# Optimization experiments

Measured on AMD Instinct MI355X. Metric: run time of the kernel, lower is better.

## Reference

```python
import jax, jax.numpy as jnp
import numpy as np

N_NODES = 100000
N_EDGES = 1600000


def _graph_conv(num_nodes, edge_index, feat, w, b, in_feats, out_feats):
    src, dst = edge_index[0], edge_index[1]
    # degree of source endpoints, clamp(min=1)^-0.5
    deg = jax.ops.segment_sum(jnp.ones_like(src, dtype=jnp.float32), src, num_segments=num_nodes)
    norm = jnp.power(jnp.clip(deg, 1.0), -0.5)[:, None]  # [N,1]
    feat = feat * norm
    if in_feats > out_feats:
        feat = feat @ w                                   # [N,out]
        rst = jax.ops.segment_sum(feat[src], dst, num_segments=num_nodes)
    else:
        rst = jax.ops.segment_sum(feat[src], dst, num_segments=num_nodes)
        rst = rst @ w
    rst = rst * norm + b
    return jax.nn.relu(rst)


def setup_inputs() -> dict:
    key = jax.random.key(0)
    ks = jax.random.split(key, 8)
    features = jax.random.normal(ks[0], (N_NODES, 256), dtype=jnp.float32)
    e_subgraph = jax.random.randint(ks[1], (2, N_EDGES), 0, N_NODES, dtype=jnp.int64 if jax.config.jax_enable_x64 else jnp.int32)
    n_subgraph = jnp.zeros((N_NODES,), dtype=jnp.int32)
    to_fetch = jax.random.randint(ks[2], (16,), 0, N_NODES, dtype=jnp.int32)
    # GraphConv weights (xavier-like scale), Linear weight (out,in) per F.linear
    w1 = jax.random.normal(ks[3], (256, 128), dtype=jnp.float32) * (2.0 / (256 + 128)) ** 0.5
    b1 = jnp.zeros((128,), dtype=jnp.float32)
    w2 = jax.random.normal(ks[4], (128, 128), dtype=jnp.float32) * (2.0 / (128 + 128)) ** 0.5
    b2 = jnp.zeros((128,), dtype=jnp.float32)
    w3 = jax.random.normal(ks[5], (16, 128), dtype=jnp.float32) * (2.0 / 128) ** 0.5
    b3 = jnp.zeros((16,), dtype=jnp.float32)
    return {"n_subgraph": n_subgraph, "e_subgraph": e_subgraph, "to_fetch": to_fetch,
            "features": features, "w1": w1, "b1": b1, "w2": w2, "b2": b2, "w3": w3, "b3": b3}


def reference(n_subgraph, e_subgraph, to_fetch, features, w1, b1, w2, b2, w3, b3):
    num_nodes = n_subgraph.shape[0]
    h = features.astype(jnp.float32)
    h = _graph_conv(num_nodes, e_subgraph, h, w1, b1, 256, 128)
    h = _graph_conv(num_nodes, e_subgraph, h, w2, b2, 128, 128)
    h = h @ w3.T + b3  # F.linear
    return (h, h)
```

## Files before the change

kernel.cpp:

```cpp
#include <hip/hip_runtime.h>

#define AP 40
#define H2P 136
#define HB 240
#define PB 240
#define NPB 256
#define NBUKMAX 512
#define CAPE 8192

typedef short bf16x8 __attribute__((ext_vector_type(8)));
typedef float f32x4 __attribute__((ext_vector_type(4)));

static __device__ __forceinline__ ushort f2bf(float f) {
  unsigned u = __float_as_uint(f);
  unsigned r = (u + 0x7fffu + ((u >> 16) & 1u)) >> 16;
  return (ushort)r;
}
static __device__ __forceinline__ float bflo(unsigned u) { return __uint_as_float(u << 16); }
static __device__ __forceinline__ float bfhi(unsigned u) { return __uint_as_float(u & 0xffff0000u); }
static __device__ __forceinline__ unsigned packbf(float lo, float hi) {
  return (unsigned)f2bf(lo) | ((unsigned)f2bf(hi) << 16);
}

__global__ __launch_bounds__(256) void k_hist(const int* __restrict__ src, int E,
                                              unsigned* __restrict__ planes, int HW) {
  __shared__ unsigned lds[25600];
  const int per = (E + HB - 1) / HB;
  const int s0 = blockIdx.x * per;
  const int s1 = min(E, s0 + per);
  for (int i = threadIdx.x; i < HW; i += 256) lds[i] = 0u;
  __syncthreads();
  for (int j = s0 + threadIdx.x; j < s1; j += 256) {
    int k = src[j];
    atomicAdd(&lds[k >> 2], 1u << ((k & 3) * 8));
  }
  __syncthreads();
  unsigned* out = planes + (size_t)blockIdx.x * HW;
  for (int i = threadIdx.x; i < HW; i += 256) out[i] = lds[i];
}

__global__ void k_hist_reduce(const unsigned* __restrict__ planes, int HW,
                              float* __restrict__ nrm, int N) {
  int w = blockIdx.x * blockDim.x + threadIdx.x;
  if (w >= HW) return;
  const unsigned* base = planes + w;
  unsigned c0 = 0, c1 = 0, c2 = 0, c3 = 0;
  for (int b = 0; b < HB; b++) {
    unsigned u = base[(size_t)b * HW];
    c0 += u & 255u; c1 += (u >> 8) & 255u; c2 += (u >> 16) & 255u; c3 += u >> 24;
  }
  int n0 = w * 4;
  unsigned c[4] = {c0, c1, c2, c3};
#pragma unroll
  for (int j = 0; j < 4; j++)
    if (n0 + j < N) {
      float d = (float)c[j];
      if (d < 1.f) d = 1.f;
      nrm[n0 + j] = 1.f / sqrtf(d);
    }
}

__global__ __launch_bounds__(256) void k_p0_hist(const int* __restrict__ dst, int E,
                                                 int* __restrict__ hist) {
  __shared__ int cnt[NBUKMAX];
  for (int i = threadIdx.x; i < NBUKMAX; i += 256) cnt[i] = 0;
  __syncthreads();
  const int per = (E + PB - 1) / PB;
  const int s0 = blockIdx.x * per;
  const int s1 = min(E, s0 + per);
  for (int j = s0 + threadIdx.x; j < s1; j += 256)
    atomicAdd(&cnt[dst[j] >> 8], 1);
  __syncthreads();
  for (int i = threadIdx.x; i < NBUKMAX; i += 256) hist[i * PB + blockIdx.x] = cnt[i];
}

__global__ __launch_bounds__(NBUKMAX) void k_p0_scan(int* __restrict__ hist) {
  __shared__ int s[NBUKMAX];
  int b = threadIdx.x;
  const int bi = b * PB;
  int tot = 0;
  for (int blk = 0; blk < PB; blk++) tot += hist[bi + blk];
  s[b] = tot;
  __syncthreads();
  for (int o = 1; o < NBUKMAX; o <<= 1) {
    int x = (b >= o) ? s[b - o] : 0;
    __syncthreads();
    s[b] += x;
    __syncthreads();
  }
  int base = s[b] - tot;
  for (int blk = 0; blk < PB; blk++) {
    int t = hist[bi + blk];
    hist[bi + blk] = base;
    base += t;
  }
}

__global__ __launch_bounds__(256) void k_p1_scatter(const int* __restrict__ src,
                                                    const int* __restrict__ dst, int E,
                                                    const int* __restrict__ hist,
                                                    int2* __restrict__ pairs) {
  __shared__ int cur[NBUKMAX];
  for (int i = threadIdx.x; i < NBUKMAX; i += 256) cur[i] = hist[i * PB + blockIdx.x];
  __syncthreads();
  const int per = (E + PB - 1) / PB;
  const int s0 = blockIdx.x * per;
  const int s1 = min(E, s0 + per);
  for (int j = s0 + threadIdx.x; j < s1; j += 256) {
    int d = dst[j];
    int pos = atomicAdd(&cur[d >> 8], 1);
    pairs[pos] = make_int2(src[j], d);
  }
}

__global__ __launch_bounds__(256) void k_p2_place(const int2* __restrict__ pairs,
                                                  const int* __restrict__ hist,
                                                  int* __restrict__ csr,
                                                  int* __restrict__ row_start,
                                                  int N, int E) {
  __shared__ int stage[CAPE];
  __shared__ int cnt[NPB];
  __shared__ int scn[NPB];
  const int b = blockIdx.x;
  const int t = threadIdx.x;
  const int n0 = b << 8;
  const int n1 = min(N, n0 + NPB);
  const int nn = n1 - n0;
  const int e0 = hist[b * PB];
  const int e1 = hist[(b + 1) * PB];
  for (int i = t; i < nn; i += 256) cnt[i] = 0;
  __syncthreads();
  for (int j = e0 + t; j < e1; j += 256) atomicAdd(&cnt[pairs[j].y - n0], 1);
  __syncthreads();
  int v = (t < nn) ? cnt[t] : 0;
  scn[t] = v;
  __syncthreads();
  for (int o = 1; o < NPB; o <<= 1) {
    int x = (t >= o) ? scn[t - o] : 0;
    __syncthreads();
    scn[t] += x;
    __syncthreads();
  }
  int excl = scn[t] - v;
  if (t < nn) row_start[n0 + t] = e0 + excl;
  if (t == NPB - 1 && n1 == N) row_start[N] = e0 + scn[t];
  __syncthreads();
  if (t < nn) cnt[t] = excl;
  __syncthreads();
  const int seg = e1 - e0;
  if (seg <= CAPE) {
    for (int j = e0 + t; j < e1; j += 256) {
      int2 pr = pairs[j];
      int rpos = atomicAdd(&cnt[pr.y - n0], 1);
      stage[rpos] = pr.x;
    }
    __syncthreads();
    for (int j = t; j < seg; j += 256) csr[e0 + j] = stage[j];
  } else {
    for (int j = e0 + t; j < e1; j += 256) {
      int2 pr = pairs[j];
      int rpos = atomicAdd(&cnt[pr.y - n0], 1);
      csr[e0 + rpos] = pr.x;
    }
  }
}

__global__ void k_cvt_all(const float* __restrict__ w1, const float* __restrict__ w2,
                          const float* __restrict__ w3, ushort* __restrict__ w1T,
                          ushort* __restrict__ w2T, ushort* __restrict__ w3b) {
  int i = blockIdx.x * blockDim.x + threadIdx.x;
  if (i < 32768) {
    int c = i >> 8, k = i & 255;
    w1T[i] = f2bf(w1[k * 128 + c]);
  } else if (i < 49152) {
    int j = i - 32768;
    int c = j >> 7, k = j & 127;
    w2T[j] = f2bf(w2[k * 128 + c]);
  } else if (i < 51200) {
    int j = i - 49152;
    w3b[j] = f2bf(w3[j]);
  }
}

__global__ __launch_bounds__(256) void k_gemm1_mfma(const float* __restrict__ feat,
                                                    const ushort* __restrict__ w1T,
                                                    const float* __restrict__ nrm,
                                                    ushort* __restrict__ Xb, int N) {
  __shared__ ushort As[128 * AP];
  __shared__ ushort Bs[128 * AP];
  const int tid = threadIdx.x;
  const int row0 = blockIdx.x * 128;
  const int wv = tid >> 6, lane = tid & 63;
  const int rbase = wv * 32;
  const int lr = lane & 15;
  const int kl = (lane >> 4) * 8;

  f32x4 acc[8][2];
#pragma unroll
  for (int ni = 0; ni < 8; ni++)
#pragma unroll
    for (int mi = 0; mi < 2; mi++) acc[ni][mi] = (f32x4)0.f;

  for (int k0 = 0; k0 < 256; k0 += 32) {
    __syncthreads();
#pragma unroll
    for (int j = 0; j < 4; j++) {
      int e = (tid + j * 256) * 4;
      int r = e >> 5, k = e & 31;
      int gr = row0 + r;
      float4 v = make_float4(0.f, 0.f, 0.f, 0.f);
      if (gr < N) v = *(const float4*)&feat[(size_t)gr * 256 + k0 + k];
      ushort4 u;
      u.x = f2bf(v.x); u.y = f2bf(v.y); u.z = f2bf(v.z); u.w = f2bf(v.w);
      *(ushort4*)&As[r * AP + k] = u;
    }
#pragma unroll
    for (int j = 0; j < 4; j++) {
      int e = (tid + j * 256) * 4;
      int c = e >> 5, k = e & 31;
      ushort4 v = *(const ushort4*)&w1T[(size_t)c * 256 + k0 + k];
      *(ushort4*)&Bs[c * AP + k] = v;
    }
    __syncthreads();
    bf16x8 bfrag[2], afrag[8];
#pragma unroll
    for (int mi = 0; mi < 2; mi++)
      bfrag[mi] = *(const bf16x8*)&As[(rbase + mi * 16 + lr) * AP + kl];
#pragma unroll
    for (int ni = 0; ni < 8; ni++)
      afrag[ni] = *(const bf16x8*)&Bs[(ni * 16 + lr) * AP + kl];
#pragma unroll
    for (int ni = 0; ni < 8; ni++)
#pragma unroll
      for (int mi = 0; mi < 2; mi++)
        acc[ni][mi] = __builtin_amdgcn_mfma_f32_16x16x32_bf16(afrag[ni], bfrag[mi], acc[ni][mi], 0, 0, 0);
  }
#pragma unroll
  for (int mi = 0; mi < 2; mi++) {
    int gr = row0 + rbase + mi * 16 + lr;
    if (gr < N) {
      float nv = nrm[gr];
#pragma unroll
      for (int ni = 0; ni < 8; ni++) {
        int c0 = ni * 16 + (lane >> 4) * 4;
        ushort4 u;
        u.x = f2bf(acc[ni][mi][0] * nv);
        u.y = f2bf(acc[ni][mi][1] * nv);
        u.z = f2bf(acc[ni][mi][2] * nv);
        u.w = f2bf(acc[ni][mi][3] * nv);
        *(ushort4*)&Xb[(size_t)gr * 128 + c0] = u;
      }
    }
  }
}

__global__ __launch_bounds__(256) void k_agg_bf(const ushort* __restrict__ Xin,
                                                const int* __restrict__ rs,
                                                const int* __restrict__ csr,
                                                const float* __restrict__ nrm,
                                                const float* __restrict__ bias,
                                                ushort* __restrict__ Out, int N, int fused) {
  const int wv = threadIdx.x >> 6, lane = threadIdx.x & 63;
  const int d = blockIdx.x * 4 + wv;
  if (d >= N) return;
  const unsigned* X = (const unsigned*)Xin;
  int s0 = rs[d], s1 = rs[d + 1];
  float a0 = 0.f, a1 = 0.f;
  int j = s0;
  for (; j + 4 <= s1; j += 4) {
    int i0 = csr[j], i1 = csr[j + 1], i2 = csr[j + 2], i3 = csr[j + 3];
    unsigned u0 = X[(size_t)i0 * 64 + lane];
    unsigned u1 = X[(size_t)i1 * 64 + lane];
    unsigned u2 = X[(size_t)i2 * 64 + lane];
    unsigned u3 = X[(size_t)i3 * 64 + lane];
    a0 += (bflo(u0) + bflo(u1)) + (bflo(u2) + bflo(u3));
    a1 += (bfhi(u0) + bfhi(u1)) + (bfhi(u2) + bfhi(u3));
  }
  for (; j < s1; j++) {
    unsigned u = X[(size_t)csr[j] * 64 + lane];
    a0 += bflo(u);
    a1 += bfhi(u);
  }
  unsigned o;
  if (fused) {
    float nv = nrm[d];
    float2 b = *(const float2*)&bias[lane * 2];
    float h0 = fmaxf(a0 * nv + b.x, 0.f) * nv;
    float h1 = fmaxf(a1 * nv + b.y, 0.f) * nv;
    o = packbf(h0, h1);
  } else {
    o = packbf(a0, a1);
  }
  ((unsigned*)Out)[(size_t)d * 64 + lane] = o;
}

__global__ __launch_bounds__(256) void k_gemm23_mfma(const ushort* __restrict__ Agg2,
                                                     const float* __restrict__ nrm,
                                                     const ushort* __restrict__ w2T,
                                                     const float* __restrict__ b2,
                                                     const ushort* __restrict__ w3b,
                                                     const float* __restrict__ b3,
                                                     float* __restrict__ out, int N) {
  __shared__ __align__(16) char lds_raw[128 * H2P * 2];
  ushort* As = (ushort*)lds_raw;
  ushort* Bs = As + 128 * AP;
  ushort* h2s = (ushort*)lds_raw;

  const int tid = threadIdx.x;
  const int row0 = blockIdx.x * 128;
  const int wv = tid >> 6, lane = tid & 63;
  const int rbase = wv * 32;
  const int lr = lane & 15;
  const int kl = (lane >> 4) * 8;

  f32x4 acc[8][2];
#pragma unroll
  for (int ni = 0; ni < 8; ni++)
#pragma unroll
    for (int mi = 0; mi < 2; mi++) acc[ni][mi] = (f32x4)0.f;

  for (int k0 = 0; k0 < 128; k0 += 32) {
    __syncthreads();
#pragma unroll
    for (int j = 0; j < 4; j++) {
      int e = (tid + j * 256) * 4;
      int r = e >> 5, k = e & 31;
      int gr = row0 + r;
      ushort4 v = make_ushort4(0, 0, 0, 0);
      if (gr < N) v = *(const ushort4*)&Agg2[(size_t)gr * 128 + k0 + k];
      *(ushort4*)&As[r * AP + k] = v;
    }
#pragma unroll
    for (int j = 0; j < 4; j++) {
      int e = (tid + j * 256) * 4;
      int c = e >> 5, k = e & 31;
      ushort4 v = *(const ushort4*)&w2T[(size_t)c * 128 + k0 + k];
      *(ushort4*)&Bs[c * AP + k] = v;
    }
    __syncthreads();
    bf16x8 bfrag[2], afrag[8];
#pragma unroll
    for (int mi = 0; mi < 2; mi++)
      bfrag[mi] = *(const bf16x8*)&As[(rbase + mi * 16 + lr) * AP + kl];
#pragma unroll
    for (int ni = 0; ni < 8; ni++)
      afrag[ni] = *(const bf16x8*)&Bs[(ni * 16 + lr) * AP + kl];
#pragma unroll
    for (int ni = 0; ni < 8; ni++)
#pragma unroll
      for (int mi = 0; mi < 2; mi++)
        acc[ni][mi] = __builtin_amdgcn_mfma_f32_16x16x32_bf16(afrag[ni], bfrag[mi], acc[ni][mi], 0, 0, 0);
  }
  __syncthreads();

#pragma unroll
  for (int mi = 0; mi < 2; mi++) {
    int r = rbase + mi * 16 + lr;
    int gr = row0 + r;
    float nv = (gr < N) ? nrm[gr] : 0.f;
#pragma unroll
    for (int ni = 0; ni < 8; ni++) {
      int c0 = ni * 16 + (lane >> 4) * 4;
      float4 bb = *(const float4*)&b2[c0];
      ushort4 u;
      u.x = f2bf(fmaxf(acc[ni][mi][0] * nv + bb.x, 0.f));
      u.y = f2bf(fmaxf(acc[ni][mi][1] * nv + bb.y, 0.f));
      u.z = f2bf(fmaxf(acc[ni][mi][2] * nv + bb.z, 0.f));
      u.w = f2bf(fmaxf(acc[ni][mi][3] * nv + bb.w, 0.f));
      *(ushort4*)&h2s[r * H2P + c0] = u;
    }
  }
  f32x4 acc3[2];
  acc3[0] = (f32x4)0.f;
  acc3[1] = (f32x4)0.f;
#pragma unroll
  for (int ks = 0; ks < 4; ks++) {
    bf16x8 a3 = *(const bf16x8*)&w3b[(size_t)lr * 128 + ks * 32 + kl];
#pragma unroll
    for (int mi = 0; mi < 2; mi++) {
      bf16x8 b3f = *(const bf16x8*)&h2s[(rbase + mi * 16 + lr) * H2P + ks * 32 + kl];
      acc3[mi] = __builtin_amdgcn_mfma_f32_16x16x32_bf16(a3, b3f, acc3[mi], 0, 0, 0);
    }
  }
#pragma unroll
  for (int mi = 0; mi < 2; mi++) {
    int gr = row0 + rbase + mi * 16 + lr;
    if (gr < N) {
      int o0 = (lane >> 4) * 4;
      float4 bb = *(const float4*)&b3[o0];
      float4 v;
      v.x = acc3[mi][0] + bb.x;
      v.y = acc3[mi][1] + bb.y;
      v.z = acc3[mi][2] + bb.z;
      v.w = acc3[mi][3] + bb.w;
      *(float4*)&out[(size_t)gr * 16 + o0] = v;
      *(float4*)&out[(size_t)(N + gr) * 16 + o0] = v;
    }
  }
}

extern "C" void kernel_launch(void* const* d_in, const int* in_sizes, int n_in,
                              void* d_out, int out_size, void* d_ws, size_t ws_size,
                              hipStream_t stream) {
  const int N = in_sizes[0];
  const int E = in_sizes[1] / 2;
  const int HW = (N + 3) / 4;
  const int NBUK = (N + NPB - 1) / NPB;

  const int* e_sub = (const int*)d_in[1];
  const int* src = e_sub;
  const int* dst = e_sub + E;
  const float* feat = (const float*)d_in[3];
  const float* w1 = (const float*)d_in[4];
  const float* b1 = (const float*)d_in[5];
  const float* w2 = (const float*)d_in[6];
  const float* b2 = (const float*)d_in[7];
  const float* w3 = (const float*)d_in[8];
  const float* b3 = (const float*)d_in[9];
  float* out = (float*)d_out;

  char* p = (char*)d_ws;
  auto alloc = [&](size_t bytes) { void* r = (void*)p; p += (bytes + 255) & ~(size_t)255; return r; };
  int* row_start = (int*)alloc((size_t)(N + 1) * 4);
  int* csr = (int*)alloc((size_t)E * 4);
  int* hist = (int*)alloc((size_t)(NBUKMAX + 1) * PB * 4);
  int2* pairs = (int2*)alloc((size_t)E * 8);
  float* nrm = (float*)alloc((size_t)N * 4);
  ushort* w1T = (ushort*)alloc((size_t)128 * 256 * 2);
  ushort* w2T = (ushort*)alloc((size_t)128 * 128 * 2);
  ushort* w3b = (ushort*)alloc((size_t)16 * 128 * 2);
  ushort* Xb = (ushort*)alloc((size_t)N * 128 * 2);
  ushort* Hb = (ushort*)alloc((size_t)N * 128 * 2);
  unsigned* planes = (unsigned*)alloc((size_t)HB * HW * 4);

  k_hist<<<HB, 256, 0, stream>>>(src, E, planes, HW);
  k_hist_reduce<<<(HW + 255) / 256, 256, 0, stream>>>(planes, HW, nrm, N);
  k_p0_hist<<<PB, 256, 0, stream>>>(dst, E, hist);
  k_p0_scan<<<1, NBUKMAX, 0, stream>>>(hist);
  k_p1_scatter<<<PB, 256, 0, stream>>>(src, dst, E, hist, pairs);
  k_p2_place<<<NBUK, 256, 0, stream>>>(pairs, hist, csr, row_start, N, E);
  k_cvt_all<<<200, 256, 0, stream>>>(w1, w2, w3, w1T, w2T, w3b);
  k_gemm1_mfma<<<(N + 127) / 128, 256, 0, stream>>>(feat, w1T, nrm, Xb, N);
  k_agg_bf<<<(N + 3) / 4, 256, 0, stream>>>(Xb, row_start, csr, nrm, b1, Hb, N, 1);
  k_agg_bf<<<(N + 3) / 4, 256, 0, stream>>>(Hb, row_start, csr, nrm, b1, Xb, N, 0);
  k_gemm23_mfma<<<(N + 127) / 128, 256, 0, stream>>>(Xb, nrm, w2T, b2, w3b, b3, out, N);
}
```

Baseline: 323.4 us.

## Fuse preprocessing kernels, pack edge pairs to 32 bits, widen gather unroll

Merges the source-degree histogram with the destination bucket histogram into one pass and halves the block count. It folds the degree reduction and the weight conversion into one launch. Edge pairs are packed into one 32-bit word (src<<8 | low dst byte) to halve scatter traffic. The aggregation gather is unrolled to 8 loads in flight, and planes and outputs use nontemporal stores and loads. Fewer blocks means less parallelism in the histogram and scatter, and the larger per-block share raises the risk of 8-bit count overflow on skewed graphs.

New measurement: 323.7 us. No clear change (+0.1%).

```diff
diff --git a/kernel.cpp b/kernel.cpp
--- a/kernel.cpp
+++ b/kernel.cpp
@@ -2,8 +2,7 @@
 
 #define AP 40
 #define H2P 136
-#define HB 240
-#define PB 240
+#define PB 120
 #define NPB 256
 #define NBUKMAX 512
 #define CAPE 8192
@@ -22,56 +21,66 @@
   return (unsigned)f2bf(lo) | ((unsigned)f2bf(hi) << 16);
 }
 
-__global__ __launch_bounds__(256) void k_hist(const int* __restrict__ src, int E,
-                                              unsigned* __restrict__ planes, int HW) {
+__global__ __launch_bounds__(256) void k_hist2(const int* __restrict__ src,
+                                               const int* __restrict__ dst, int E,
+                                               unsigned* __restrict__ planes, int HW,
+                                               int* __restrict__ hist) {
   __shared__ unsigned lds[25600];
-  const int per = (E + HB - 1) / HB;
+  __shared__ int cnt[NBUKMAX];
+  const int per = (E + PB - 1) / PB;
   const int s0 = blockIdx.x * per;
   const int s1 = min(E, s0 + per);
   for (int i = threadIdx.x; i < HW; i += 256) lds[i] = 0u;
+  for (int i = threadIdx.x; i < NBUKMAX; i += 256) cnt[i] = 0;
   __syncthreads();
   for (int j = s0 + threadIdx.x; j < s1; j += 256) {
     int k = src[j];
     atomicAdd(&lds[k >> 2], 1u << ((k & 3) * 8));
+    atomicAdd(&cnt[dst[j] >> 8], 1);
   }
   __syncthreads();
   unsigned* out = planes + (size_t)blockIdx.x * HW;
-  for (int i = threadIdx.x; i < HW; i += 256) out[i] = lds[i];
-}
-
-__global__ void k_hist_reduce(const unsigned* __restrict__ planes, int HW,
-                              float* __restrict__ nrm, int N) {
-  int w = blockIdx.x * blockDim.x + threadIdx.x;
-  if (w >= HW) return;
-  const unsigned* base = planes + w;
-  unsigned c0 = 0, c1 = 0, c2 = 0, c3 = 0;
-  for (int b = 0; b < HB; b++) {
-    unsigned u = base[(size_t)b * HW];
-    c0 += u & 255u; c1 += (u >> 8) & 255u; c2 += (u >> 16) & 255u; c3 += u >> 24;
-  }
-  int n0 = w * 4;
-  unsigned c[4] = {c0, c1, c2, c3};
-#pragma unroll
-  for (int j = 0; j < 4; j++)
-    if (n0 + j < N) {
-      float d = (float)c[j];
-      if (d < 1.f) d = 1.f;
-      nrm[n0 + j] = 1.f / sqrtf(d);
-    }
-}
-
-__global__ __launch_bounds__(256) void k_p0_hist(const int* __restrict__ dst, int E,
-                                                 int* __restrict__ hist) {
-  __shared__ int cnt[NBUKMAX];
-  for (int i = threadIdx.x; i < NBUKMAX; i += 256) cnt[i] = 0;
-  __syncthreads();
-  const int per = (E + PB - 1) / PB;
-  const int s0 = blockIdx.x * per;
-  const int s1 = min(E, s0 + per);
-  for (int j = s0 + threadIdx.x; j < s1; j += 256)
-    atomicAdd(&cnt[dst[j] >> 8], 1);
-  __syncthreads();
+  for (int i = threadIdx.x; i < HW; i += 256) __builtin_nontemporal_store(lds[i], &out[i]);
   for (int i = threadIdx.x; i < NBUKMAX; i += 256) hist[i * PB + blockIdx.x] = cnt[i];
+}
+
+__global__ void k_reduce_cvt(const unsigned* __restrict__ planes, int HW,
+                             float* __restrict__ nrm, int N, int nrb,
+                             const float* __restrict__ w1, const float* __restrict__ w2,
+                             const float* __restrict__ w3, ushort* __restrict__ w1T,
+                             ushort* __restrict__ w2T, ushort* __restrict__ w3b) {
+  if ((int)blockIdx.x < nrb) {
+    int w = blockIdx.x * 256 + threadIdx.x;
+    if (w >= HW) return;
+    const unsigned* base = planes + w;
+    unsigned c0 = 0, c1 = 0, c2 = 0, c3 = 0;
+    for (int b = 0; b < PB; b++) {
+      unsigned u = __builtin_nontemporal_load(&base[(size_t)b * HW]);
+      c0 += u & 255u; c1 += (u >> 8) & 255u; c2 += (u >> 16) & 255u; c3 += u >> 24;
+    }
+    int n0 = w * 4;
+    unsigned c[4] = {c0, c1, c2, c3};
+#pragma unroll
+    for (int j = 0; j < 4; j++)
+      if (n0 + j < N) {
+        float d = (float)c[j];
+        if (d < 1.f) d = 1.f;
+        nrm[n0 + j] = 1.f / sqrtf(d);
+      }
+  } else {
+    int i = (blockIdx.x - nrb) * 256 + threadIdx.x;
+    if (i < 32768) {
+      int c = i >> 8, k = i & 255;
+      w1T[i] = f2bf(w1[k * 128 + c]);
+    } else if (i < 49152) {
+      int j = i - 32768;
+      int c = j >> 7, k = j & 127;
+      w2T[j] = f2bf(w2[k * 128 + c]);
+    } else if (i < 51200) {
+      int j = i - 49152;
+      w3b[j] = f2bf(w3[j]);
+    }
+  }
 }
 
 __global__ __launch_bounds__(NBUKMAX) void k_p0_scan(int* __restrict__ hist) {
@@ -99,7 +108,7 @@
 __global__ __launch_bounds__(256) void k_p1_scatter(const int* __restrict__ src,
                                                     const int* __restrict__ dst, int E,
                                                     const int* __restrict__ hist,
-                                                    int2* __restrict__ pairs) {
+                                                    unsigned* __restrict__ pairs) {
   __shared__ int cur[NBUKMAX];
   for (int i = threadIdx.x; i < NBUKMAX; i += 256) cur[i] = hist[i * PB + blockIdx.x];
   __syncthreads();
@@ -109,11 +118,11 @@
   for (int j = s0 + threadIdx.x; j < s1; j += 256) {
     int d = dst[j];
     int pos = atomicAdd(&cur[d >> 8], 1);
-    pairs[pos] = make_int2(src[j], d);
-  }
-}
-
-__global__ __launch_bounds__(256) void k_p2_place(const int2* __restrict__ pairs,
+    pairs[pos] = ((unsigned)src[j] << 8) | (unsigned)(d & 255);
+  }
+}
+
+__global__ __launch_bounds__(256) void k_p2_place(const unsigned* __restrict__ pairs,
                                                   const int* __restrict__ hist,
                                                   int* __restrict__ csr,
                                                   int* __restrict__ row_start,
@@ -130,7 +139,7 @@
   const int e1 = hist[(b + 1) * PB];
   for (int i = t; i < nn; i += 256) cnt[i] = 0;
   __syncthreads();
-  for (int j = e0 + t; j < e1; j += 256) atomicAdd(&cnt[pairs[j].y - n0], 1);
+  for (int j = e0 + t; j < e1; j += 256) atomicAdd(&cnt[pairs[j] & 255u], 1);
   __syncthreads();
   int v = (t < nn) ? cnt[t] : 0;
   scn[t] = v;
@@ -150,35 +159,18 @@
   const int seg = e1 - e0;
   if (seg <= CAPE) {
     for (int j = e0 + t; j < e1; j += 256) {
-      int2 pr = pairs[j];
-      int rpos = atomicAdd(&cnt[pr.y - n0], 1);
-      stage[rpos] = pr.x;
+      unsigned pr = pairs[j];
+      int rpos = atomicAdd(&cnt[pr & 255u], 1);
+      stage[rpos] = (int)(pr >> 8);
     }
     __syncthreads();
     for (int j = t; j < seg; j += 256) csr[e0 + j] = stage[j];
   } else {
     for (int j = e0 + t; j < e1; j += 256) {
-      int2 pr = pairs[j];
-      int rpos = atomicAdd(&cnt[pr.y - n0], 1);
-      csr[e0 + rpos] = pr.x;
-    }
-  }
-}
-
-__global__ void k_cvt_all(const float* __restrict__ w1, const float* __restrict__ w2,
-                          const float* __restrict__ w3, ushort* __restrict__ w1T,
-                          ushort* __restrict__ w2T, ushort* __restrict__ w3b) {
-  int i = blockIdx.x * blockDim.x + threadIdx.x;
-  if (i < 32768) {
-    int c = i >> 8, k = i & 255;
-    w1T[i] = f2bf(w1[k * 128 + c]);
-  } else if (i < 49152) {
-    int j = i - 32768;
-    int c = j >> 7, k = j & 127;
-    w2T[j] = f2bf(w2[k * 128 + c]);
-  } else if (i < 51200) {
-    int j = i - 49152;
-    w3b[j] = f2bf(w3[j]);
+      unsigned pr = pairs[j];
+      int rpos = atomicAdd(&cnt[pr & 255u], 1);
+      csr[e0 + rpos] = (int)(pr >> 8);
+    }
   }
 }
 
@@ -267,14 +259,15 @@
   int s0 = rs[d], s1 = rs[d + 1];
   float a0 = 0.f, a1 = 0.f;
   int j = s0;
-  for (; j + 4 <= s1; j += 4) {
-    int i0 = csr[j], i1 = csr[j + 1], i2 = csr[j + 2], i3 = csr[j + 3];
-    unsigned u0 = X[(size_t)i0 * 64 + lane];
-    unsigned u1 = X[(size_t)i1 * 64 + lane];
-    unsigned u2 = X[(size_t)i2 * 64 + lane];
-    unsigned u3 = X[(size_t)i3 * 64 + lane];
-    a0 += (bflo(u0) + bflo(u1)) + (bflo(u2) + bflo(u3));
-    a1 += (bfhi(u0) + bfhi(u1)) + (bfhi(u2) + bfhi(u3));
+  for (; j + 8 <= s1; j += 8) {
+    int idx[8];
+#pragma unroll
+    for (int q = 0; q < 8; q++) idx[q] = csr[j + q];
+    unsigned u[8];
+#pragma unroll
+    for (int q = 0; q < 8; q++) u[q] = X[(size_t)idx[q] * 64 + lane];
+#pragma unroll
+    for (int q = 0; q < 8; q++) { a0 += bflo(u[q]); a1 += bfhi(u[q]); }
   }
   for (; j < s1; j++) {
     unsigned u = X[(size_t)csr[j] * 64 + lane];
@@ -291,7 +284,7 @@
   } else {
     o = packbf(a0, a1);
   }
-  ((unsigned*)Out)[(size_t)d * 64 + lane] = o;
+  __builtin_nontemporal_store(o, &((unsigned*)Out)[(size_t)d * 64 + lane]);
 }
 
 __global__ __launch_bounds__(256) void k_gemm23_mfma(const ushort* __restrict__ Agg2,
@@ -406,6 +399,7 @@
   const int E = in_sizes[1] / 2;
   const int HW = (N + 3) / 4;
   const int NBUK = (N + NPB - 1) / NPB;
+  const int nrb = (HW + 255) / 256;
 
   const int* e_sub = (const int*)d_in[1];
   const int* src = e_sub;
@@ -424,22 +418,20 @@
   int* row_start = (int*)alloc((size_t)(N + 1) * 4);
   int* csr = (int*)alloc((size_t)E * 4);
   int* hist = (int*)alloc((size_t)(NBUKMAX + 1) * PB * 4);
-  int2* pairs = (int2*)alloc((size_t)E * 8);
+  unsigned* pairs = (unsigned*)alloc((size_t)E * 4);
   float* nrm = (float*)alloc((size_t)N * 4);
   ushort* w1T = (ushort*)alloc((size_t)128 * 256 * 2);
   ushort* w2T = (ushort*)alloc((size_t)128 * 128 * 2);
   ushort* w3b = (ushort*)alloc((size_t)16 * 128 * 2);
   ushort* Xb = (ushort*)alloc((size_t)N * 128 * 2);
   ushort* Hb = (ushort*)alloc((size_t)N * 128 * 2);
-  unsigned* planes = (unsigned*)alloc((size_t)HB * HW * 4);
-
-  k_hist<<<HB, 256, 0, stream>>>(src, E, planes, HW);
-  k_hist_reduce<<<(HW + 255) / 256, 256, 0, stream>>>(planes, HW, nrm, N);
-  k_p0_hist<<<PB, 256, 0, stream>>>(dst, E, hist);
+  unsigned* planes = (unsigned*)alloc((size_t)PB * HW * 4);
+
+  k_hist2<<<PB, 256, 0, stream>>>(src, dst, E, planes, HW, hist);
+  k_reduce_cvt<<<nrb + 200, 256, 0, stream>>>(planes, HW, nrm, N, nrb, w1, w2, w3, w1T, w2T, w3b);
   k_p0_scan<<<1, NBUKMAX, 0, stream>>>(hist);
   k_p1_scatter<<<PB, 256, 0, stream>>>(src, dst, E, hist, pairs);
   k_p2_place<<<NBUK, 256, 0, stream>>>(pairs, hist, csr, row_start, N, E);
-  k_cvt_all<<<200, 256, 0, stream>>>(w1, w2, w3, w1T, w2T, w3b);
   k_gemm1_mfma<<<(N + 127) / 128, 256, 0, stream>>>(feat, w1T, nrm, Xb, N);
   k_agg_bf<<<(N + 3) / 4, 256, 0, stream>>>(Xb, row_start, csr, nrm, b1, Hb, N, 1);
   k_agg_bf<<<(N + 3) / 4, 256, 0, stream>>>(Hb, row_start, csr, nrm, b1, Xb, N, 0);
```
